# Optimization experiments

Hardware: AMD Instinct MI355X
Metric: run time of the kernel (lower is better)

Reference implementation:

```python
import jax, jax.numpy as jnp
import numpy as np

NUM_CLASSES = 4
LAMBDA_CREDA = 1.0
LAMBDA_ENTROPY = 0.1
SIGMA = 32.0          # config.sigma (fixed, not 'auto')
USE_UNCERTAINTY = True
EPS = 1e-8
LOG2 = float(np.log(2.0))

N_S, N_T, D = 4096, 4096, 1024


def _rbf(x, y, sigma):
    # squared euclidean distances (== torch.cdist(x,y)**2), then gaussian kernel
    d2 = (jnp.sum(x * x, axis=1)[:, None] + jnp.sum(y * y, axis=1)[None, :]
          - 2.0 * (x @ y.T))
    d2 = jnp.maximum(d2, 0.0)
    return jnp.exp(-d2 / (2.0 * sigma * sigma + EPS))


def _h2(tr, sumsq):
    # H2(A) = -log2(tr(A@A)), A = K/(tr(K)+eps); tr(A@A) = sum(K*K)/(tr+eps)^2 for symmetric K
    info = sumsq / (tr + EPS) ** 2
    return -jnp.log(info + EPS) / LOG2


def setup_inputs() -> dict:
    key = jax.random.key(0)
    k1, k2, k3, k4, k5 = jax.random.split(key, 5)
    return {
        "features_s": jax.random.normal(k1, (N_S, D), dtype=jnp.float32),
        "logits_s": jax.random.normal(k2, (N_S, NUM_CLASSES), dtype=jnp.float32),
        "features_t": jax.random.normal(k3, (N_T, D), dtype=jnp.float32),
        "logits_t": jax.random.normal(k4, (N_T, NUM_CLASSES), dtype=jnp.float32),
        "labels_s": jax.random.randint(k5, (N_S,), 0, NUM_CLASSES, dtype=jnp.int32),
    }


def reference(features_s, logits_s, features_t, logits_t, labels_s):
    # ---- classification loss (cross entropy on source) ----
    logp_s = jax.nn.log_softmax(logits_s, axis=1)
    loss_cls = -jnp.mean(jnp.take_along_axis(logp_s, labels_s[:, None], axis=1))

    # ---- target entropy loss ----
    probs_t = jax.nn.softmax(logits_t, axis=1)
    loss_ent = -jnp.mean(jnp.sum(probs_t * jnp.log(probs_t + EPS), axis=1))

    # ---- pseudo labels + uncertainty weights ----
    pseudo_t = jnp.argmax(jax.lax.stop_gradient(probs_t), axis=1)
    if USE_UNCERTAINTY:
        h2_probs = -jnp.log(jnp.sum(probs_t ** 2, axis=1) + EPS) / LOG2
        h2_max = np.log(float(NUM_CLASSES)) / LOG2
        w = 1.0 - h2_probs / (h2_max + EPS)          # [N_t]
    else:
        w = jnp.ones((features_t.shape[0],), dtype=probs_t.dtype)

    # ---- shared RBF kernel blocks (sigma fixed -> identical across classes) ----
    K_ss = _rbf(features_s, features_s, SIGMA)       # [N_s, N_s]
    K_tt = _rbf(features_t, features_t, SIGMA)       # [N_t, N_t]
    K_st = _rbf(features_s, features_t, SIGMA)       # [N_s, N_t]

    # per-class masks (zero-masking a kernel preserves trace and trace(K@K))
    Ms = jax.nn.one_hot(labels_s, NUM_CLASSES, dtype=K_ss.dtype).T   # [C, N_s]
    Mt = jax.nn.one_hot(pseudo_t, NUM_CLASSES, dtype=K_tt.dtype).T   # [C, N_t]
    Wt = Mt * w[None, :]                                             # [C, N_t]
    Wt2 = Wt * Wt

    n_s = jnp.sum(Ms, axis=1)                        # class counts (source)
    n_t = jnp.sum(Mt, axis=1)                        # class counts (target)

    # traces: diag(K)=1, target block weighted by outer(w,w)
    tr_s = n_s                                       # [C]
    tr_t = jnp.sum(Wt2, axis=1)                      # [C]

    # sum of squared entries of the masked (and weighted) blocks
    ss_s = jnp.einsum('ci,ci->c', Ms @ (K_ss ** 2), Ms)     # tr(K_s^2) per class
    ss_t = jnp.einsum('ci,ci->c', Wt2 @ (K_tt ** 2), Wt2)   # tr(K_tw^2) per class
    ss_st = jnp.einsum('ci,ci->c', Ms @ (K_st ** 2), Mt)    # sum(K_st^2) per class

    h_s = _h2(tr_s, ss_s)
    h_t = _h2(tr_t, ss_t)
    h_mix = _h2(tr_s + tr_t, ss_s + 2.0 * ss_st + ss_t)

    per_class = h_mix - 0.5 * (h_s + h_t)            # [C]
    valid = (n_s >= 2) & (n_t >= 2)
    n_valid = jnp.sum(valid.astype(per_class.dtype))
    creda_sum = jnp.sum(jnp.where(valid, per_class, 0.0))
    loss_creda = jnp.where(n_valid > 0, creda_sum / jnp.maximum(n_valid, 1.0), 0.0)

    total_loss = loss_cls + LAMBDA_CREDA * loss_creda + LAMBDA_ENTROPY * loss_ent
    return total_loss
```

## Files before the change

kernel.cpp:

```cpp
#include <hip/hip_runtime.h>
#include <cstdint>
#include <cstddef>

#define NS_ROWS 4096
#define NT_ROWS 4096
#define DIM 1024
#define NC 4
#define NWORK_MAX 2432
#define ACC_N 26

typedef __attribute__((ext_vector_type(4))) float f32x4;
typedef long long i64;

#define GLOBAL_AS __attribute__((address_space(1)))
#define LDS_AS __attribute__((address_space(3)))


__device__ __forceinline__ int argmax4(float4 l) {
    int am = 0; float bm = l.x;
    if (l.y > bm) { bm = l.y; am = 1; }
    if (l.z > bm) { bm = l.z; am = 2; }
    if (l.w > bm) { bm = l.w; am = 3; }
    return am;
}

__global__ __launch_bounds__(1024)
void rank_prep(const int* __restrict__ labels, const float* __restrict__ LS,
               const float* __restrict__ LT,
               int* __restrict__ ctrl, float* __restrict__ acc,
               int* __restrict__ dstS, int* __restrict__ dstT) {
    __shared__ unsigned long long wtot[16];
    __shared__ float wred[16];
    __shared__ float cls4[NC];
    int t = threadIdx.x;
    int wid = t >> 6, lane = t & 63;
    bool isS = (blockIdx.x == 0);
    int* dst = isS ? dstS : dstT;
    const float EPSF = 1e-8f;
    const float INV_LOG2 = 1.44269504088896340736f;

    if (t < NC) cls4[t] = 0.f;

    int c4[4];
    float localScalar = 0.f;
    float localW2[NC] = {0.f, 0.f, 0.f, 0.f};
    if (isS) {
        int4 lab4 = ((const int4*)labels)[t];
        c4[0] = lab4.x; c4[1] = lab4.y; c4[2] = lab4.z; c4[3] = lab4.w;
#pragma unroll
        for (int i = 0; i < 4; ++i) {
            float4 l = ((const float4*)LS)[t * 4 + i];
            float m = fmaxf(fmaxf(l.x, l.y), fmaxf(l.z, l.w));
            float e = expf(l.x - m) + expf(l.y - m) + expf(l.z - m) + expf(l.w - m);
            float lse = m + logf(e);
            int lab = c4[i];
            float ll = (lab == 0) ? l.x : (lab == 1) ? l.y : (lab == 2) ? l.z : l.w;
            localScalar += lse - ll;
        }
    } else {
#pragma unroll
        for (int i = 0; i < 4; ++i) {
            float4 l = ((const float4*)LT)[t * 4 + i];
            int am = argmax4(l);
            c4[i] = am;
            float m = fmaxf(fmaxf(l.x, l.y), fmaxf(l.z, l.w));
            float p0 = expf(l.x - m), p1 = expf(l.y - m),
                  p2 = expf(l.z - m), p3 = expf(l.w - m);
            float s = p0 + p1 + p2 + p3;
            p0 /= s; p1 /= s; p2 /= s; p3 /= s;
            localScalar += p0 * logf(p0 + EPSF) + p1 * logf(p1 + EPSF) +
                           p2 * logf(p2 + EPSF) + p3 * logf(p3 + EPSF);
            float sumsq = p0 * p0 + p1 * p1 + p2 * p2 + p3 * p3;
            float h2 = -logf(sumsq + EPSF) * INV_LOG2;
            float w = 1.0f - h2 / (2.0f + EPSF);
            localW2[am] += w * w;
        }
    }

    unsigned long long packed = 0ULL;
#pragma unroll
    for (int i = 0; i < 4; ++i) packed += 1ULL << (c4[i] * 16);
    unsigned long long v = packed;
#pragma unroll
    for (int off = 1; off < 64; off <<= 1) {
        unsigned long long n = __shfl_up(v, off);
        if (lane >= off) v += n;
    }
    if (lane == 63) wtot[wid] = v;
    __syncthreads();
    if (t < 16) {
        unsigned long long x = wtot[t];
#pragma unroll
        for (int off = 1; off < 16; off <<= 1) {
            unsigned long long n = __shfl_up(x, off);
            if (lane >= off) x += n;
        }
        wtot[t] = x;
    }
    __syncthreads();
    unsigned long long incl = v + (wid > 0 ? wtot[wid - 1] : 0ULL);
    unsigned long long tot = wtot[15];
    unsigned long long ex = incl - packed;

    int baseC[NC]; int b = 0;
#pragma unroll
    for (int c = 0; c < NC; ++c) {
        baseC[c] = b;
        b += (int)((tot >> (c * 16)) & 0xFFFFULL);
    }
    if (t == 0) {
#pragma unroll
        for (int c = 0; c < NC; ++c) {
            ctrl[(isS ? 0 : 4) + c] = (int)((tot >> (c * 16)) & 0xFFFFULL);
            ctrl[(isS ? 16 : 20) + c] = baseC[c];
        }
    }
    int pref[NC];
#pragma unroll
    for (int c = 0; c < NC; ++c)
        pref[c] = (int)((ex >> (c * 16)) & 0xFFFFULL) + baseC[c];
#pragma unroll
    for (int i = 0; i < 4; ++i) {
        int c = c4[i];
        dst[t * 4 + i] = pref[c]++;
    }

    for (int off = 32; off; off >>= 1) localScalar += __shfl_xor(localScalar, off);
    if (lane == 0) wred[wid] = localScalar;
    if (!isS) {
#pragma unroll
        for (int c = 0; c < NC; ++c) {
            float x = localW2[c];
            for (int off = 32; off; off >>= 1) x += __shfl_xor(x, off);
            if (lane == 0 && x != 0.f) atomicAdd(&cls4[c], x);
        }
    }
    __syncthreads();
    if (t == 0) {
        float s = 0.f;
        for (int i = 0; i < 16; ++i) s += wred[i];
        acc[isS ? 0 : 1] = s;
    }
    if (!isS && t < NC) acc[10 + t] = cls4[t];
}

__global__ void scatter_aux(const float* __restrict__ FS, const float* __restrict__ FT,
                            const int* __restrict__ labels, const float* __restrict__ LT,
                            const int* __restrict__ dstS, const int* __restrict__ dstT,
                            unsigned char* __restrict__ fs, unsigned char* __restrict__ ft,
                            float* __restrict__ nS, float* __restrict__ wS, int* __restrict__ cS,
                            float* __restrict__ nT, float* __restrict__ wT, int* __restrict__ cT,
                            int* __restrict__ ctrl, int4* __restrict__ wl,
                            float* __restrict__ acc) {
    if (blockIdx.x == 2048) {
        int t = threadIdx.x;
        if (t >= 12 && t < 24) acc[14 + (t - 12)] = 0.f;
        int Ts[NC], Tt[NC];
#pragma unroll
        for (int c = 0; c < NC; ++c) {
            Ts[c] = (ctrl[c] + 127) >> 7;
            Tt[c] = (ctrl[4 + c] + 127) >> 7;
        }
        int segSize[12];
#pragma unroll
        for (int c = 0; c < NC; ++c) {
            segSize[c * 3 + 0] = Ts[c] * (Ts[c] + 1) / 2;
            segSize[c * 3 + 1] = Tt[c] * (Tt[c] + 1) / 2;
            segSize[c * 3 + 2] = Ts[c] * Tt[c];
        }
        if (t == 31) {
            int n = 0;
            for (int s = 0; s < 12; ++s) n += segSize[s];
            ctrl[24] = n;
        }
        if (t >= 12) return;
        int base = 0;
        for (int s = 0; s < t; ++s) base += segSize[s];
        int c = t / 3, kind = t % 3;
        int4* w = wl + base;
        int n = 0;
        if (kind == 0) {
            for (int tj = 0; tj < Ts[c]; ++tj)
                for (int ti = 0; ti <= tj; ++ti) w[n++] = make_int4(0, c, ti, tj);
        } else if (kind == 1) {
            for (int tj = 0; tj < Tt[c]; ++tj)
                for (int ti = 0; ti <= tj; ++ti) w[n++] = make_int4(1, c, ti, tj);
        } else {
            for (int ti = 0; ti < Ts[c]; ++ti)
                for (int tj = 0; tj < Tt[c]; ++tj) w[n++] = make_int4(2, c, ti, tj);
        }
        return;
    }

    int row = blockIdx.x * 4 + (threadIdx.x >> 6);
    int lane = threadIdx.x & 63;
    bool isS = row < NS_ROWS;
    int r = isS ? row : row - NS_ROWS;
    int dst = isS ? dstS[r] : dstT[r];

    const float* src = (isS ? FS : FT) + (size_t)r * DIM;
    float4 v0 = ((const float4*)src)[lane * 4 + 0];
    float4 v1 = ((const float4*)src)[lane * 4 + 1];
    float4 v2 = ((const float4*)src)[lane * 4 + 2];
    float4 v3 = ((const float4*)src)[lane * 4 + 3];
    int w0 = 0, w1 = 0, w2 = 0, w3 = 0;
    w0 = __builtin_amdgcn_cvt_pk_fp8_f32(v0.x, v0.y, w0, false);
    w0 = __builtin_amdgcn_cvt_pk_fp8_f32(v0.z, v0.w, w0, true);
    w1 = __builtin_amdgcn_cvt_pk_fp8_f32(v1.x, v1.y, w1, false);
    w1 = __builtin_amdgcn_cvt_pk_fp8_f32(v1.z, v1.w, w1, true);
    w2 = __builtin_amdgcn_cvt_pk_fp8_f32(v2.x, v2.y, w2, false);
    w2 = __builtin_amdgcn_cvt_pk_fp8_f32(v2.z, v2.w, w2, true);
    w3 = __builtin_amdgcn_cvt_pk_fp8_f32(v3.x, v3.y, w3, false);
    w3 = __builtin_amdgcn_cvt_pk_fp8_f32(v3.z, v3.w, w3, true);

    float ssum = 0.f;
#define ACCQ(wv)                                                       \
    do {                                                               \
        float q0 = __builtin_amdgcn_cvt_f32_fp8((wv), 0);              \
        float q1 = __builtin_amdgcn_cvt_f32_fp8((wv), 1);              \
        float q2 = __builtin_amdgcn_cvt_f32_fp8((wv), 2);              \
        float q3 = __builtin_amdgcn_cvt_f32_fp8((wv), 3);              \
        ssum += q0 * q0 + q1 * q1 + q2 * q2 + q3 * q3;                 \
    } while (0)
    ACCQ(w0); ACCQ(w1); ACCQ(w2); ACCQ(w3);
#undef ACCQ

    unsigned char* fdst = (isS ? fs : ft) + (size_t)dst * DIM;
    *(uint4*)(fdst + lane * 16) = make_uint4((unsigned)w0, (unsigned)w1,
                                             (unsigned)w2, (unsigned)w3);

    for (int off = 32; off; off >>= 1) ssum += __shfl_xor(ssum, off);

    if (lane == 0) {
        if (isS) {
            nS[dst] = ssum; wS[dst] = 1.0f; cS[dst] = labels[r];
        } else {
            float4 l = ((const float4*)LT)[r];
            int am = argmax4(l);
            float m = fmaxf(fmaxf(l.x, l.y), fmaxf(l.z, l.w));
            float p0 = expf(l.x - m), p1 = expf(l.y - m),
                  p2 = expf(l.z - m), p3 = expf(l.w - m);
            float s = p0 + p1 + p2 + p3;
            float sumsq = (p0 * p0 + p1 * p1 + p2 * p2 + p3 * p3) / (s * s);
            const float INV_LOG2 = 1.44269504088896340736f;
            float h2 = -logf(sumsq + 1e-8f) * INV_LOG2;
            float w = 1.0f - h2 / (2.0f + 1e-8f);
            nT[dst] = ssum; wT[dst] = w * w; cT[dst] = am;
        }
    }
}

__global__ __launch_bounds__(256, 4)
void gemm_reduce(const unsigned char* __restrict__ fs, const unsigned char* __restrict__ ft,
                 const float* __restrict__ nS, const float* __restrict__ wS, const int* __restrict__ cS,
                 const float* __restrict__ nT, const float* __restrict__ wT, const int* __restrict__ cT,
                 const int* __restrict__ ctrl, const int4* __restrict__ wl,
                 float* __restrict__ acc) {
    __shared__ unsigned char As[2][128 * 64];
    __shared__ unsigned char Bs[2][128 * 64];
    __shared__ float sred;

    int nwork = ctrl[24];
    int chunk = (nwork + 7) >> 3;
    int sub = blockIdx.x >> 3, xcd = blockIdx.x & 7;
    if (sub >= chunk) return;
    int widx = xcd * chunk + sub;
    if (widx >= nwork) return;
    int4 it = wl[widx];
    int kind = it.x, cls = it.y, ti = it.z, tj = it.w;

    const unsigned char *A, *B;
    const float *nA, *nB, *wA, *wB;
    const int *cA, *cB;
    int baseA, baseB;
    if (kind == 0)      { A = fs; B = fs; nA = nS; nB = nS; wA = wS; wB = wS; cA = cS; cB = cS;
                          baseA = ctrl[16 + cls]; baseB = baseA; }
    else if (kind == 1) { A = ft; B = ft; nA = nT; nB = nT; wA = wT; wB = wT; cA = cT; cB = cT;
                          baseA = ctrl[20 + cls]; baseB = baseA; }
    else                { A = fs; B = ft; nA = nS; nB = nT; wA = wS; cA = cS; cB = cT;
                          wB = wS;
                          baseA = ctrl[16 + cls]; baseB = ctrl[20 + cls]; }
    float* outp = acc + 14 + kind * 4 + cls;
    float factor = (kind != 2 && ti != tj) ? 2.0f : 1.0f;

    int tid = threadIdx.x;
    int lane = tid & 63;
    int wid = tid >> 6;
    int wr = wid >> 1, wc = wid & 1;

    int rowA0 = baseA + ti * 128;
    int rowB0 = baseB + tj * 128;

    int srow = tid >> 2;
    int sb = (((tid & 3) ^ ((tid >> 3) & 3))) * 16;

    const unsigned char* pa0 = A + (size_t)min(rowA0 + srow,      4095) * DIM + sb;
    const unsigned char* pa1 = A + (size_t)min(rowA0 + srow + 64, 4095) * DIM + sb;
    const unsigned char* pb0 = B + (size_t)min(rowB0 + srow,      4095) * DIM + sb;
    const unsigned char* pb1 = B + (size_t)min(rowB0 + srow + 64, 4095) * DIM + sb;

    f32x4 accf[4][4];
#pragma unroll
    for (int m = 0; m < 4; ++m)
#pragma unroll
        for (int n = 0; n < 4; ++n) accf[m][n] = (f32x4)(0.f);

    int lr = lane & 15;
    int lk = (lane >> 4) * 8;
    int sw = (lr >> 1) & 3;

#define STAGE(buf, kt)                                                            \
    do {                                                                          \
        int k0_ = (kt) * 64;                                                      \
        __builtin_amdgcn_global_load_lds((const GLOBAL_AS void*)(pa0 + k0_),      \
            (LDS_AS void*)(As[buf] + tid * 16), 16, 0, 0);                        \
        __builtin_amdgcn_global_load_lds((const GLOBAL_AS void*)(pa1 + k0_),      \
            (LDS_AS void*)(As[buf] + 4096 + tid * 16), 16, 0, 0);                 \
        __builtin_amdgcn_global_load_lds((const GLOBAL_AS void*)(pb0 + k0_),      \
            (LDS_AS void*)(Bs[buf] + tid * 16), 16, 0, 0);                        \
        __builtin_amdgcn_global_load_lds((const GLOBAL_AS void*)(pb1 + k0_),      \
            (LDS_AS void*)(Bs[buf] + 4096 + tid * 16), 16, 0, 0);                 \
    } while (0)

#define COMPUTE_HALF(buf, kk)                                                     \
    do {                                                                          \
        int b_ = (kk) + lk;                                                       \
        int bs_ = ((((b_) >> 4) ^ sw) << 4) | ((b_) & 15);                        \
        i64 af[4], bfr[4];                                                        \
        _Pragma("unroll")                                                         \
        for (int f = 0; f < 4; ++f)                                               \
            af[f] = *(const i64*)(As[buf] + (wr * 64 + f * 16 + lr) * 64 + bs_);  \
        _Pragma("unroll")                                                         \
        for (int f = 0; f < 4; ++f)                                               \
            bfr[f] = *(const i64*)(Bs[buf] + (wc * 64 + f * 16 + lr) * 64 + bs_); \
        _Pragma("unroll")                                                         \
        for (int m = 0; m < 4; ++m)                                               \
            _Pragma("unroll")                                                     \
            for (int n = 0; n < 4; ++n)                                           \
                accf[m][n] = __builtin_amdgcn_mfma_f32_16x16x32_fp8_fp8(          \
                    af[m], bfr[n], accf[m][n], 0, 0, 0);                          \
    } while (0)

    STAGE(0, 0);
    asm volatile("s_waitcnt vmcnt(0)");
    __syncthreads();

    int cur = 0;
    for (int kt = 0; kt < DIM / 64 - 1; ++kt) {
        STAGE(cur ^ 1, kt + 1);
        COMPUTE_HALF(cur, 0);
        COMPUTE_HALF(cur, 32);
        __syncthreads();
        cur ^= 1;
    }
    COMPUTE_HALF(cur, 0);
    COMPUTE_HALF(cur, 32);

    int rowBase = rowA0 + wr * 64;
    int colBase = rowB0 + wc * 64;

    float cn[4], cw[4];
#pragma unroll
    for (int f = 0; f < 4; ++f) {
        int gj = colBase + f * 16 + lr;
        int gjc = min(gj, 4095);
        cn[f] = nB[gjc];
        cw[f] = (gj < 4096 && cB[gjc] == cls) ? wB[gjc] : 0.0f;
    }

    const float NEGF = (-2.0f / (2.0f * 32.0f * 32.0f + 1e-8f)) * 1.44269504088896340736f;
    float lacc = 0.f;

#pragma unroll
    for (int m = 0; m < 4; ++m) {
#pragma unroll
        for (int j = 0; j < 4; ++j) {
            int gi = rowBase + m * 16 + (lane >> 4) * 4 + j;
            int gic = min(gi, 4095);
            float rn = nA[gic];
            float rw = (gi < 4096 && cA[gic] == cls) ? wA[gic] : 0.0f;
#pragma unroll
            for (int n = 0; n < 4; ++n) {
                float dot = accf[m][n][j];
                float d2 = rn + cn[n] - 2.0f * dot;
                d2 = fmaxf(d2, 0.0f);
                float k2 = exp2f(d2 * NEGF);
                lacc += k2 * rw * cw[n];
            }
        }
    }

    if (tid == 0) sred = 0.f;
    __syncthreads();
    for (int off = 32; off; off >>= 1) lacc += __shfl_xor(lacc, off);
    if (lane == 0) atomicAdd(&sred, lacc);
    __syncthreads();
    if (tid == 0) atomicAdd(outp, factor * sred);
#undef STAGE
#undef COMPUTE_HALF
}

__global__ void finalize_kernel(const float* __restrict__ acc, const int* __restrict__ ctrl,
                                float* __restrict__ out) {
    if (threadIdx.x != 0 || blockIdx.x != 0) return;
    const double EPS = 1e-8;
    const double LOG2 = 0.6931471805599453;
    double loss_cls = (double)acc[0] / NS_ROWS;
    double loss_ent = -(double)acc[1] / NT_ROWS;
    double creda_sum = 0.0, n_valid = 0.0;
    for (int c = 0; c < NC; ++c) {
        int nsc_i = ctrl[c], ntc_i = ctrl[4 + c];
        double trt = acc[10 + c];
        double sss = acc[14 + c], sst = acc[18 + c], ssst = acc[22 + c];
        double trs = (double)nsc_i;
        double info_s = sss / ((trs + EPS) * (trs + EPS));
        double h_s = -log(info_s + EPS) / LOG2;
        double info_t = sst / ((trt + EPS) * (trt + EPS));
        double h_t = -log(info_t + EPS) / LOG2;
        double trm = trs + trt;
        double ssm = sss + 2.0 * ssst + sst;
        double info_m = ssm / ((trm + EPS) * (trm + EPS));
        double h_m = -log(info_m + EPS) / LOG2;
        double pc = h_m - 0.5 * (h_s + h_t);
        if (nsc_i >= 2 && ntc_i >= 2) { creda_sum += pc; n_valid += 1.0; }
    }
    double creda = (n_valid > 0.0) ? creda_sum / n_valid : 0.0;
    out[0] = (float)(loss_cls + 1.0 * creda + 0.1 * loss_ent);
}

extern "C" void kernel_launch(void* const* d_in, const int* in_sizes, int n_in,
                              void* d_out, int out_size, void* d_ws, size_t ws_size,
                              hipStream_t stream) {
    const float* FS = (const float*)d_in[0];
    const float* LS = (const float*)d_in[1];
    const float* FT = (const float*)d_in[2];
    const float* LT = (const float*)d_in[3];
    const int* LAB = (const int*)d_in[4];

    char* ws = (char*)d_ws;
    unsigned char* fs = (unsigned char*)(ws);
    unsigned char* ft = (unsigned char*)(ws + 4194304);
    char* p = ws + 8388608;
    float* nS  = (float*)(p);
    float* wS  = (float*)(p + 16384);
    int*   cS  = (int*)  (p + 32768);
    float* nT  = (float*)(p + 49152);
    float* wT  = (float*)(p + 65536);
    int*   cT  = (int*)  (p + 81920);
    int*   ctrl = (int*)  (p + 98304);
    float* acc  = (float*)(p + 98304 + 128);
    int4*  wl   = (int4*) (p + 98304 + 512);
    int*   dstS = (int*)  (p + 98304 + 512 + NWORK_MAX * 16);
    int*   dstT = dstS + NS_ROWS;

    rank_prep<<<2, 1024, 0, stream>>>(LAB, LS, LT, ctrl, acc, dstS, dstT);
    scatter_aux<<<2049, 256, 0, stream>>>(FS, FT, LAB, LT, dstS, dstT, fs, ft,
                                          nS, wS, cS, nT, wT, cT, ctrl, wl, acc);
    gemm_reduce<<<NWORK_MAX, 256, 0, stream>>>(fs, ft, nS, wS, cS, nT, wT, cT,
                                               ctrl, wl, acc);
    finalize_kernel<<<1, 1, 0, stream>>>(acc, ctrl, (float*)d_out);
}
```

Before: 62.01 us.

## Shrink GEMM tiles to 64x64 and add grid-stride work loop

```diff
diff --git a/kernel.cpp b/kernel.cpp
--- a/kernel.cpp
+++ b/kernel.cpp
@@ -6,7 +6,8 @@
 #define NT_ROWS 4096
 #define DIM 1024
 #define NC 4
-#define NWORK_MAX 2432
+#define GRID_B 2432
+#define NWORK_MAX 8448
 #define ACC_N 26
 
 typedef __attribute__((ext_vector_type(4))) float f32x4;
@@ -158,8 +159,8 @@
         int Ts[NC], Tt[NC];
 #pragma unroll
         for (int c = 0; c < NC; ++c) {
-            Ts[c] = (ctrl[c] + 127) >> 7;
-            Tt[c] = (ctrl[4 + c] + 127) >> 7;
+            Ts[c] = (ctrl[c] + 63) >> 6;
+            Tt[c] = (ctrl[4 + c] + 63) >> 6;
         }
         int segSize[12];
 #pragma unroll
@@ -250,154 +251,156 @@
     }
 }
 
-__global__ __launch_bounds__(256, 4)
+__global__ __launch_bounds__(256, 8)
 void gemm_reduce(const unsigned char* __restrict__ fs, const unsigned char* __restrict__ ft,
                  const float* __restrict__ nS, const float* __restrict__ wS, const int* __restrict__ cS,
                  const float* __restrict__ nT, const float* __restrict__ wT, const int* __restrict__ cT,
                  const int* __restrict__ ctrl, const int4* __restrict__ wl,
                  float* __restrict__ acc) {
-    __shared__ unsigned char As[2][128 * 64];
-    __shared__ unsigned char Bs[2][128 * 64];
+    __shared__ unsigned char As[2][64 * 64];
+    __shared__ unsigned char Bs[2][64 * 64];
     __shared__ float sred;
 
     int nwork = ctrl[24];
-    int chunk = (nwork + 7) >> 3;
-    int sub = blockIdx.x >> 3, xcd = blockIdx.x & 7;
-    if (sub >= chunk) return;
-    int widx = xcd * chunk + sub;
-    if (widx >= nwork) return;
-    int4 it = wl[widx];
-    int kind = it.x, cls = it.y, ti = it.z, tj = it.w;
-
-    const unsigned char *A, *B;
-    const float *nA, *nB, *wA, *wB;
-    const int *cA, *cB;
-    int baseA, baseB;
-    if (kind == 0)      { A = fs; B = fs; nA = nS; nB = nS; wA = wS; wB = wS; cA = cS; cB = cS;
-                          baseA = ctrl[16 + cls]; baseB = baseA; }
-    else if (kind == 1) { A = ft; B = ft; nA = nT; nB = nT; wA = wT; wB = wT; cA = cT; cB = cT;
-                          baseA = ctrl[20 + cls]; baseB = baseA; }
-    else                { A = fs; B = ft; nA = nS; nB = nT; wA = wS; cA = cS; cB = cT;
-                          wB = wS;
-                          baseA = ctrl[16 + cls]; baseB = ctrl[20 + cls]; }
-    float* outp = acc + 14 + kind * 4 + cls;
-    float factor = (kind != 2 && ti != tj) ? 2.0f : 1.0f;
+    int start;
+    if (nwork <= GRID_B) {
+        int chunk = (nwork + 7) >> 3;
+        int sub = blockIdx.x >> 3, xcd = blockIdx.x & 7;
+        if (sub >= chunk) return;
+        start = xcd * chunk + sub;
+        if (start >= nwork) return;
+    } else {
+        start = blockIdx.x;
+    }
 
     int tid = threadIdx.x;
     int lane = tid & 63;
     int wid = tid >> 6;
     int wr = wid >> 1, wc = wid & 1;
-
-    int rowA0 = baseA + ti * 128;
-    int rowB0 = baseB + tj * 128;
-
-    int srow = tid >> 2;
-    int sb = (((tid & 3) ^ ((tid >> 3) & 3))) * 16;
-
-    const unsigned char* pa0 = A + (size_t)min(rowA0 + srow,      4095) * DIM + sb;
-    const unsigned char* pa1 = A + (size_t)min(rowA0 + srow + 64, 4095) * DIM + sb;
-    const unsigned char* pb0 = B + (size_t)min(rowB0 + srow,      4095) * DIM + sb;
-    const unsigned char* pb1 = B + (size_t)min(rowB0 + srow + 64, 4095) * DIM + sb;
-
-    f32x4 accf[4][4];
-#pragma unroll
-    for (int m = 0; m < 4; ++m)
-#pragma unroll
-        for (int n = 0; n < 4; ++n) accf[m][n] = (f32x4)(0.f);
-
     int lr = lane & 15;
     int lk = (lane >> 4) * 8;
     int sw = (lr >> 1) & 3;
+    int srow = tid >> 2;
+    int sb = (((tid & 3) ^ ((tid >> 3) & 3))) * 16;
+
+    for (int widx = start; widx < nwork; widx += GRID_B) {
+        int4 it = wl[widx];
+        int kind = it.x, cls = it.y, ti = it.z, tj = it.w;
+
+        const unsigned char *A, *B;
+        const float *nA, *nB, *wA, *wB;
+        const int *cA, *cB;
+        int baseA, baseB;
+        if (kind == 0)      { A = fs; B = fs; nA = nS; nB = nS; wA = wS; wB = wS; cA = cS; cB = cS;
+                              baseA = ctrl[16 + cls]; baseB = baseA; }
+        else if (kind == 1) { A = ft; B = ft; nA = nT; nB = nT; wA = wT; wB = wT; cA = cT; cB = cT;
+                              baseA = ctrl[20 + cls]; baseB = baseA; }
+        else                { A = fs; B = ft; nA = nS; nB = nT; wA = wS; cA = cS; cB = cT;
+                              wB = wS;
+                              baseA = ctrl[16 + cls]; baseB = ctrl[20 + cls]; }
+        float* outp = acc + 14 + kind * 4 + cls;
+        float factor = (kind != 2 && ti != tj) ? 2.0f : 1.0f;
+
+        int rowA0 = baseA + ti * 64;
+        int rowB0 = baseB + tj * 64;
+
+        const unsigned char* pa = A + (size_t)min(rowA0 + srow, 4095) * DIM + sb;
+        const unsigned char* pb = B + (size_t)min(rowB0 + srow, 4095) * DIM + sb;
+
+        f32x4 accf[2][2];
+#pragma unroll
+        for (int m = 0; m < 2; ++m)
+#pragma unroll
+            for (int n = 0; n < 2; ++n) accf[m][n] = (f32x4)(0.f);
 
 #define STAGE(buf, kt)                                                            \
-    do {                                                                          \
-        int k0_ = (kt) * 64;                                                      \
-        __builtin_amdgcn_global_load_lds((const GLOBAL_AS void*)(pa0 + k0_),      \
-            (LDS_AS void*)(As[buf] + tid * 16), 16, 0, 0);                        \
-        __builtin_amdgcn_global_load_lds((const GLOBAL_AS void*)(pa1 + k0_),      \
-            (LDS_AS void*)(As[buf] + 4096 + tid * 16), 16, 0, 0);                 \
-        __builtin_amdgcn_global_load_lds((const GLOBAL_AS void*)(pb0 + k0_),      \
-            (LDS_AS void*)(Bs[buf] + tid * 16), 16, 0, 0);                        \
-        __builtin_amdgcn_global_load_lds((const GLOBAL_AS void*)(pb1 + k0_),      \
-            (LDS_AS void*)(Bs[buf] + 4096 + tid * 16), 16, 0, 0);                 \
-    } while (0)
+        do {                                                                      \
+            int k0_ = (kt) * 64;                                                  \
+            __builtin_amdgcn_global_load_lds((const GLOBAL_AS void*)(pa + k0_),   \
+                (LDS_AS void*)(As[buf] + tid * 16), 16, 0, 0);                    \
+            __builtin_amdgcn_global_load_lds((const GLOBAL_AS void*)(pb + k0_),   \
+                (LDS_AS void*)(Bs[buf] + tid * 16), 16, 0, 0);                    \
+        } while (0)
 
 #define COMPUTE_HALF(buf, kk)                                                     \
-    do {                                                                          \
-        int b_ = (kk) + lk;                                                       \
-        int bs_ = ((((b_) >> 4) ^ sw) << 4) | ((b_) & 15);                        \
-        i64 af[4], bfr[4];                                                        \
-        _Pragma("unroll")                                                         \
-        for (int f = 0; f < 4; ++f)                                               \
-            af[f] = *(const i64*)(As[buf] + (wr * 64 + f * 16 + lr) * 64 + bs_);  \
-        _Pragma("unroll")                                                         \
-        for (int f = 0; f < 4; ++f)                                               \
-            bfr[f] = *(const i64*)(Bs[buf] + (wc * 64 + f * 16 + lr) * 64 + bs_); \
-        _Pragma("unroll")                                                         \
-        for (int m = 0; m < 4; ++m)                                               \
+        do {                                                                      \
+            int b_ = (kk) + lk;                                                   \
+            int bs_ = ((((b_) >> 4) ^ sw) << 4) | ((b_) & 15);                    \
+            i64 af[2], bfr[2];                                                    \
             _Pragma("unroll")                                                     \
-            for (int n = 0; n < 4; ++n)                                           \
-                accf[m][n] = __builtin_amdgcn_mfma_f32_16x16x32_fp8_fp8(          \
-                    af[m], bfr[n], accf[m][n], 0, 0, 0);                          \
-    } while (0)
-
-    STAGE(0, 0);
-    asm volatile("s_waitcnt vmcnt(0)");
-    __syncthreads();
-
-    int cur = 0;
-    for (int kt = 0; kt < DIM / 64 - 1; ++kt) {
-        STAGE(cur ^ 1, kt + 1);
+            for (int f = 0; f < 2; ++f)                                           \
+                af[f] = *(const i64*)(As[buf] + (wr * 32 + f * 16 + lr) * 64 + bs_); \
+            _Pragma("unroll")                                                     \
+            for (int f = 0; f < 2; ++f)                                           \
+                bfr[f] = *(const i64*)(Bs[buf] + (wc * 32 + f * 16 + lr) * 64 + bs_); \
+            _Pragma("unroll")                                                     \
+            for (int m = 0; m < 2; ++m)                                           \
+                _Pragma("unroll")                                                 \
+                for (int n = 0; n < 2; ++n)                                       \
+                    accf[m][n] = __builtin_amdgcn_mfma_f32_16x16x32_fp8_fp8(      \
+                        af[m], bfr[n], accf[m][n], 0, 0, 0);                      \
+        } while (0)
+
+        STAGE(0, 0);
+        asm volatile("s_waitcnt vmcnt(0)");
+        __syncthreads();
+
+        int cur = 0;
+        for (int kt = 0; kt < DIM / 64 - 1; ++kt) {
+            STAGE(cur ^ 1, kt + 1);
+            COMPUTE_HALF(cur, 0);
+            COMPUTE_HALF(cur, 32);
+            __syncthreads();
+            cur ^= 1;
+        }
         COMPUTE_HALF(cur, 0);
         COMPUTE_HALF(cur, 32);
+
+        int rowBase = rowA0 + wr * 32;
+        int colBase = rowB0 + wc * 32;
+
+        float cn[2], cw[2];
+#pragma unroll
+        for (int f = 0; f < 2; ++f) {
+            int gj = colBase + f * 16 + lr;
+            int gjc = min(gj, 4095);
+            cn[f] = nB[gjc];
+            cw[f] = (gj < 4096 && cB[gjc] == cls) ? wB[gjc] : 0.0f;
+        }
+
+        const float NEGF = (-2.0f / (2.0f * 32.0f * 32.0f + 1e-8f)) * 1.44269504088896340736f;
+        float lacc = 0.f;
+
+#pragma unroll
+        for (int m = 0; m < 2; ++m) {
+#pragma unroll
+            for (int j = 0; j < 4; ++j) {
+                int gi = rowBase + m * 16 + (lane >> 4) * 4 + j;
+                int gic = min(gi, 4095);
+                float rn = nA[gic];
+                float rw = (gi < 4096 && cA[gic] == cls) ? wA[gic] : 0.0f;
+#pragma unroll
+                for (int n = 0; n < 2; ++n) {
+                    float dot = accf[m][n][j];
+                    float d2 = rn + cn[n] - 2.0f * dot;
+                    d2 = fmaxf(d2, 0.0f);
+                    float k2 = exp2f(d2 * NEGF);
+                    lacc += k2 * rw * cw[n];
+                }
+            }
+        }
+
+        if (tid == 0) sred = 0.f;
         __syncthreads();
-        cur ^= 1;
-    }
-    COMPUTE_HALF(cur, 0);
-    COMPUTE_HALF(cur, 32);
-
-    int rowBase = rowA0 + wr * 64;
-    int colBase = rowB0 + wc * 64;
-
-    float cn[4], cw[4];
-#pragma unroll
-    for (int f = 0; f < 4; ++f) {
-        int gj = colBase + f * 16 + lr;
-        int gjc = min(gj, 4095);
-        cn[f] = nB[gjc];
-        cw[f] = (gj < 4096 && cB[gjc] == cls) ? wB[gjc] : 0.0f;
-    }
-
-    const float NEGF = (-2.0f / (2.0f * 32.0f * 32.0f + 1e-8f)) * 1.44269504088896340736f;
-    float lacc = 0.f;
-
-#pragma unroll
-    for (int m = 0; m < 4; ++m) {
-#pragma unroll
-        for (int j = 0; j < 4; ++j) {
-            int gi = rowBase + m * 16 + (lane >> 4) * 4 + j;
-            int gic = min(gi, 4095);
-            float rn = nA[gic];
-            float rw = (gi < 4096 && cA[gic] == cls) ? wA[gic] : 0.0f;
-#pragma unroll
-            for (int n = 0; n < 4; ++n) {
-                float dot = accf[m][n][j];
-                float d2 = rn + cn[n] - 2.0f * dot;
-                d2 = fmaxf(d2, 0.0f);
-                float k2 = exp2f(d2 * NEGF);
-                lacc += k2 * rw * cw[n];
-            }
-        }
-    }
-
-    if (tid == 0) sred = 0.f;
-    __syncthreads();
-    for (int off = 32; off; off >>= 1) lacc += __shfl_xor(lacc, off);
-    if (lane == 0) atomicAdd(&sred, lacc);
-    __syncthreads();
-    if (tid == 0) atomicAdd(outp, factor * sred);
+        for (int off = 32; off; off >>= 1) lacc += __shfl_xor(lacc, off);
+        if (lane == 0) atomicAdd(&sred, lacc);
+        __syncthreads();
+        if (tid == 0) atomicAdd(outp, factor * sred);
+        if (nwork <= GRID_B) break;
+        __syncthreads();
 #undef STAGE
 #undef COMPUTE_HALF
+    }
 }
 
 __global__ void finalize_kernel(const float* __restrict__ acc, const int* __restrict__ ctrl,
@@ -456,7 +459,7 @@
     rank_prep<<<2, 1024, 0, stream>>>(LAB, LS, LT, ctrl, acc, dstS, dstT);
     scatter_aux<<<2049, 256, 0, stream>>>(FS, FT, LAB, LT, dstS, dstT, fs, ft,
                                           nS, wS, cS, nT, wT, cT, ctrl, wl, acc);
-    gemm_reduce<<<NWORK_MAX, 256, 0, stream>>>(fs, ft, nS, wS, cS, nT, wT, cT,
-                                               ctrl, wl, acc);
+    gemm_reduce<<<GRID_B, 256, 0, stream>>>(fs, ft, nS, wS, cS, nT, wT, cT,
+                                            ctrl, wl, acc);
     finalize_kernel<<<1, 1, 0, stream>>>(acc, ctrl, (float*)d_out);
 }
```

Measured after the change: 90.90 us. 1.47x slower.
